# Kernel optimization log

Measured on AMD Instinct MI355X. Metric: run time of the kernel, lower is better.

## Reference

```python
import jax, jax.numpy as jnp
import numpy as np
from jax.scipy.special import logsumexp

N_ITERS = 20


def setup_inputs() -> dict:
    key = jax.random.key(0)
    k1, _ = jax.random.split(key)
    cost_matrix = jax.random.uniform(k1, (64, 1024, 1024), dtype=jnp.float32)
    epsilon = jnp.ones((1,), dtype=jnp.float32)
    return {"cost_matrix": cost_matrix, "epsilon": epsilon}


def reference(cost_matrix, epsilon):
    # log-space Sinkhorn: alternate row / column normalization in log domain
    log_alpha = -cost_matrix / epsilon  # (B, N, N)

    def step(la, _):
        la = la - logsumexp(la, axis=-1, keepdims=True)  # row normalize
        la = la - logsumexp(la, axis=-2, keepdims=True)  # col normalize
        return la, None

    log_alpha, _ = jax.lax.scan(step, log_alpha, None, length=N_ITERS)
    return jnp.exp(log_alpha)
```

## Files before the change

### kernel.cpp

```cpp
#include <hip/hip_runtime.h>
#include <hip/hip_fp16.h>


#define BATCH 64
#define N 1024
#define NITERS 20
#define ROWS_PER_BLOCK 64
#define BLOCKS_PER_BATCH (N / ROWS_PER_BLOCK)
#define THREADS 256
#define NU2 (N / 4)
#define NU4 (N / 8)
#define NU4F8 (N / 16)

typedef float f32x2 __attribute__((ext_vector_type(2)));

union H2U { __half2 h; unsigned u; };

__device__ __forceinline__ float4 h4_to_f4(uint2 r) {
    H2U a, b;
    a.u = r.x; b.u = r.y;
    float2 fa = __half22float2(a.h);
    float2 fb = __half22float2(b.h);
    return make_float4(fa.x, fa.y, fb.x, fb.y);
}

__device__ __forceinline__ void h8_unpack(uint4 r, float* f) {
    H2U a, b, c, d;
    a.u = r.x; b.u = r.y; c.u = r.z; d.u = r.w;
    float2 fa = __half22float2(a.h), fb = __half22float2(b.h);
    float2 fc = __half22float2(c.h), fd = __half22float2(d.h);
    f[0] = fa.x; f[1] = fa.y; f[2] = fb.x; f[3] = fb.y;
    f[4] = fc.x; f[5] = fc.y; f[6] = fd.x; f[7] = fd.y;
}

__device__ __forceinline__ uint4 h8_pack(const float* f) {
    H2U a, b, c, d;
    a.h = __float22half2_rn(make_float2(f[0], f[1]));
    b.h = __float22half2_rn(make_float2(f[2], f[3]));
    c.h = __float22half2_rn(make_float2(f[4], f[5]));
    d.h = __float22half2_rn(make_float2(f[6], f[7]));
    uint4 r; r.x = a.u; r.y = b.u; r.z = c.u; r.w = d.u;
    return r;
}

__device__ __forceinline__ uint4 pack_fp8_16(const float* k) {
    uint4 r;
    int a;
    a = __builtin_amdgcn_cvt_pk_fp8_f32(k[0],  k[1],  0, false);
    a = __builtin_amdgcn_cvt_pk_fp8_f32(k[2],  k[3],  a, true);
    r.x = (unsigned)a;
    a = __builtin_amdgcn_cvt_pk_fp8_f32(k[4],  k[5],  0, false);
    a = __builtin_amdgcn_cvt_pk_fp8_f32(k[6],  k[7],  a, true);
    r.y = (unsigned)a;
    a = __builtin_amdgcn_cvt_pk_fp8_f32(k[8],  k[9],  0, false);
    a = __builtin_amdgcn_cvt_pk_fp8_f32(k[10], k[11], a, true);
    r.z = (unsigned)a;
    a = __builtin_amdgcn_cvt_pk_fp8_f32(k[12], k[13], 0, false);
    a = __builtin_amdgcn_cvt_pk_fp8_f32(k[14], k[15], a, true);
    r.w = (unsigned)a;
    return r;
}

__device__ __forceinline__ void unpack_fp8_16(uint4 r, float* f) {
    f32x2 p;
    p = __builtin_amdgcn_cvt_pk_f32_fp8((int)r.x, false); f[0]  = p.x; f[1]  = p.y;
    p = __builtin_amdgcn_cvt_pk_f32_fp8((int)r.x, true);  f[2]  = p.x; f[3]  = p.y;
    p = __builtin_amdgcn_cvt_pk_f32_fp8((int)r.y, false); f[4]  = p.x; f[5]  = p.y;
    p = __builtin_amdgcn_cvt_pk_f32_fp8((int)r.y, true);  f[6]  = p.x; f[7]  = p.y;
    p = __builtin_amdgcn_cvt_pk_f32_fp8((int)r.z, false); f[8]  = p.x; f[9]  = p.y;
    p = __builtin_amdgcn_cvt_pk_f32_fp8((int)r.z, true);  f[10] = p.x; f[11] = p.y;
    p = __builtin_amdgcn_cvt_pk_f32_fp8((int)r.w, false); f[12] = p.x; f[13] = p.y;
    p = __builtin_amdgcn_cvt_pk_f32_fp8((int)r.w, true);  f[14] = p.x; f[15] = p.y;
}


__global__ __launch_bounds__(THREADS) void sk_zero(float* __restrict__ csum_all) {
    const int i = blockIdx.x * THREADS + threadIdx.x;
    csum_all[i] = 0.0f;
}

__global__ __launch_bounds__(THREADS) void sk_build(
        const float* __restrict__ C, const float* __restrict__ eps,
        uint4* __restrict__ K16, uint4* __restrict__ K8,
        float* __restrict__ u, float* __restrict__ csum_out) {
    __shared__ float4 smc[4][N / 4];
    const int t = threadIdx.x;
    const int lane = t & 63, w = t >> 6;
    const int b = blockIdx.y;
    const int row0 = blockIdx.x * ROWS_PER_BLOCK + w * 16;
    const float nie = -1.0f / eps[0];

    const float4* __restrict__ Cp =
        (const float4*)(C + ((size_t)b * N + row0) * N) + lane * 4;
    uint4* __restrict__ Kp16 = K16 + ((size_t)b * N + row0) * NU4 + lane * 2;
    uint4* __restrict__ Kp8  = K8  + ((size_t)b * N + row0) * NU4F8 + lane;

    float colacc[16];
    #pragma unroll
    for (int q = 0; q < 16; ++q) colacc[q] = 0.0f;

    float4 cur[4];
    #pragma unroll
    for (int q = 0; q < 4; ++q) cur[q] = Cp[q];

    for (int i = 0; i < 16; ++i) {
        float4 nxt[4];
        if (i < 15) {
            #pragma unroll
            for (int q = 0; q < 4; ++q) nxt[q] = Cp[(i + 1) * (N / 4) + q];
        }
        float k[16];
        const float* cf = (const float*)cur;
        #pragma unroll
        for (int q = 0; q < 16; ++q) k[q] = __expf(cf[q] * nie);

        Kp16[(size_t)i * NU4]     = h8_pack(k);
        Kp16[(size_t)i * NU4 + 1] = h8_pack(k + 8);
        Kp8[(size_t)i * NU4F8]    = pack_fp8_16(k);

        float s = (((k[0] + k[1]) + (k[2] + k[3])) + ((k[4] + k[5]) + (k[6] + k[7])))
                + (((k[8] + k[9]) + (k[10] + k[11])) + ((k[12] + k[13]) + (k[14] + k[15])));
        #pragma unroll
        for (int off = 32; off; off >>= 1) s += __shfl_xor(s, off, 64);
        const float ui = 1.0f / s;
        if (lane == 0) u[b * N + row0 + i] = ui;

        #pragma unroll
        for (int q = 0; q < 16; ++q) colacc[q] += k[q] * ui;

        if (i < 15) {
            #pragma unroll
            for (int q = 0; q < 4; ++q) cur[q] = nxt[q];
        }
    }

    #pragma unroll
    for (int q = 0; q < 4; ++q)
        smc[w][lane * 4 + q] = make_float4(colacc[4 * q], colacc[4 * q + 1],
                                           colacc[4 * q + 2], colacc[4 * q + 3]);
    __syncthreads();
    float4 s0 = smc[0][t], s1 = smc[1][t], s2 = smc[2][t], s3 = smc[3][t];
    float4 sum;
    sum.x = (s0.x + s1.x) + (s2.x + s3.x);
    sum.y = (s0.y + s1.y) + (s2.y + s3.y);
    sum.z = (s0.z + s1.z) + (s2.z + s3.z);
    sum.w = (s0.w + s1.w) + (s2.w + s3.w);
    float* cs = csum_out + b * N + 4 * t;
    atomicAdd(cs + 0, sum.x);
    atomicAdd(cs + 1, sum.y);
    atomicAdd(cs + 2, sum.z);
    atomicAdd(cs + 3, sum.w);
}

__global__ __launch_bounds__(THREADS) void sk_iter8(
        const uint4* __restrict__ K8, const float* __restrict__ csum_in,
        float* __restrict__ csum_out) {
    __shared__ float4 smc[4][N / 4];
    const int t = threadIdx.x;
    const int lane = t & 63, w = t >> 6;
    const int b = blockIdx.y;
    const int row0 = blockIdx.x * ROWS_PER_BLOCK + w * 16;

    const float4* __restrict__ cin = (const float4*)(csum_in + b * N) + lane * 4;
    float vv[16];
    #pragma unroll
    for (int q = 0; q < 4; ++q) {
        float4 c = cin[q];
        vv[4 * q + 0] = 1.0f / c.x;
        vv[4 * q + 1] = 1.0f / c.y;
        vv[4 * q + 2] = 1.0f / c.z;
        vv[4 * q + 3] = 1.0f / c.w;
    }

    const uint4* __restrict__ Kp = K8 + ((size_t)b * N + row0) * NU4F8 + lane;

    float colacc[16];
    #pragma unroll
    for (int q = 0; q < 16; ++q) colacc[q] = 0.0f;

    uint4 c0 = Kp[0];
    uint4 c1 = Kp[NU4F8];
    for (int i = 0; i < 16; ++i) {
        uint4 c2;
        if (i < 14) c2 = Kp[(size_t)(i + 2) * NU4F8];

        float k[16];
        unpack_fp8_16(c0, k);

        float pa = (k[0] * vv[0] + k[1] * vv[1]) + (k[2] * vv[2] + k[3] * vv[3]);
        float pb = (k[4] * vv[4] + k[5] * vv[5]) + (k[6] * vv[6] + k[7] * vv[7]);
        float pc = (k[8] * vv[8] + k[9] * vv[9]) + (k[10] * vv[10] + k[11] * vv[11]);
        float pd = (k[12] * vv[12] + k[13] * vv[13]) + (k[14] * vv[14] + k[15] * vv[15]);
        float s = (pa + pb) + (pc + pd);

        #pragma unroll
        for (int off = 32; off; off >>= 1) s += __shfl_xor(s, off, 64);
        const float ui = 1.0f / s;

        #pragma unroll
        for (int q = 0; q < 16; ++q) colacc[q] += k[q] * ui;

        c0 = c1;
        if (i < 14) c1 = c2;
    }

    #pragma unroll
    for (int q = 0; q < 4; ++q)
        smc[w][lane * 4 + q] = make_float4(colacc[4 * q], colacc[4 * q + 1],
                                           colacc[4 * q + 2], colacc[4 * q + 3]);
    __syncthreads();
    float4 s0 = smc[0][t], s1 = smc[1][t], s2 = smc[2][t], s3 = smc[3][t];
    float4 sum;
    sum.x = (s0.x + s1.x) + (s2.x + s3.x);
    sum.y = (s0.y + s1.y) + (s2.y + s3.y);
    sum.z = (s0.z + s1.z) + (s2.z + s3.z);
    sum.w = (s0.w + s1.w) + (s2.w + s3.w);
    float* cs = csum_out + b * N + 4 * t;
    atomicAdd(cs + 0, sum.x);
    atomicAdd(cs + 1, sum.y);
    atomicAdd(cs + 2, sum.z);
    atomicAdd(cs + 3, sum.w);
}

__global__ __launch_bounds__(THREADS) void sk_iter(
        const uint4* __restrict__ K, const float* __restrict__ csum_in,
        float* __restrict__ u, float* __restrict__ csum_out) {
    __shared__ float4 smc[4][N / 4];
    const int t = threadIdx.x;
    const int lane = t & 63, w = t >> 6;
    const int b = blockIdx.y;
    const int row0 = blockIdx.x * ROWS_PER_BLOCK + w * 16;

    const float4* __restrict__ cin = (const float4*)(csum_in + b * N) + lane * 4;
    float vv[16];
    #pragma unroll
    for (int q = 0; q < 4; ++q) {
        float4 c = cin[q];
        vv[4 * q + 0] = 1.0f / c.x;
        vv[4 * q + 1] = 1.0f / c.y;
        vv[4 * q + 2] = 1.0f / c.z;
        vv[4 * q + 3] = 1.0f / c.w;
    }

    const uint4* __restrict__ Kp = K + ((size_t)b * N + row0) * NU4 + lane * 2;

    float colacc[16];
    #pragma unroll
    for (int q = 0; q < 16; ++q) colacc[q] = 0.0f;

    uint4 c0 = Kp[0], c1 = Kp[1];
    for (int i = 0; i < 16; ++i) {
        uint4 n0, n1;
        if (i < 15) {
            n0 = Kp[(size_t)(i + 1) * NU4];
            n1 = Kp[(size_t)(i + 1) * NU4 + 1];
        }
        float k[16];
        h8_unpack(c0, k);
        h8_unpack(c1, k + 8);

        float pa = (k[0] * vv[0] + k[1] * vv[1]) + (k[2] * vv[2] + k[3] * vv[3]);
        float pb = (k[4] * vv[4] + k[5] * vv[5]) + (k[6] * vv[6] + k[7] * vv[7]);
        float pc = (k[8] * vv[8] + k[9] * vv[9]) + (k[10] * vv[10] + k[11] * vv[11]);
        float pd = (k[12] * vv[12] + k[13] * vv[13]) + (k[14] * vv[14] + k[15] * vv[15]);
        float s = (pa + pb) + (pc + pd);

        #pragma unroll
        for (int off = 32; off; off >>= 1) s += __shfl_xor(s, off, 64);
        const float ui = 1.0f / s;
        if (lane == 0) u[b * N + row0 + i] = ui;

        #pragma unroll
        for (int q = 0; q < 16; ++q) colacc[q] += k[q] * ui;

        if (i < 15) { c0 = n0; c1 = n1; }
    }

    #pragma unroll
    for (int q = 0; q < 4; ++q)
        smc[w][lane * 4 + q] = make_float4(colacc[4 * q], colacc[4 * q + 1],
                                           colacc[4 * q + 2], colacc[4 * q + 3]);
    __syncthreads();
    float4 s0 = smc[0][t], s1 = smc[1][t], s2 = smc[2][t], s3 = smc[3][t];
    float4 sum;
    sum.x = (s0.x + s1.x) + (s2.x + s3.x);
    sum.y = (s0.y + s1.y) + (s2.y + s3.y);
    sum.z = (s0.z + s1.z) + (s2.z + s3.z);
    sum.w = (s0.w + s1.w) + (s2.w + s3.w);
    float* cs = csum_out + b * N + 4 * t;
    atomicAdd(cs + 0, sum.x);
    atomicAdd(cs + 1, sum.y);
    atomicAdd(cs + 2, sum.z);
    atomicAdd(cs + 3, sum.w);
}

__global__ __launch_bounds__(THREADS) void sk_final(
        const uint2* __restrict__ K, const float* __restrict__ u,
        const float* __restrict__ csum_last, float* __restrict__ out) {
    const int t = threadIdx.x;
    const int row = blockIdx.x;
    const int b = blockIdx.y;
    const float ui = u[b * N + row];
    const float4 ci = ((const float4*)(csum_last + b * N))[t];
    const float4 vv = make_float4(1.0f / ci.x, 1.0f / ci.y, 1.0f / ci.z, 1.0f / ci.w);
    const size_t base = (size_t)b * N + row;
    float4 k = h4_to_f4((K + base * NU2)[t]);
    float4 o;
    o.x = k.x * ui * vv.x;
    o.y = k.y * ui * vv.y;
    o.z = k.z * ui * vv.z;
    o.w = k.w * ui * vv.w;
    ((float4*)(out + base * N))[t] = o;
}


__device__ __forceinline__ float block_reduce_broadcast(float val, float* lds) {
    #pragma unroll
    for (int off = 32; off > 0; off >>= 1)
        val += __shfl_xor(val, off, 64);
    const int lane = threadIdx.x & 63;
    const int wid  = threadIdx.x >> 6;
    if (lane == 0) lds[wid] = val;
    __syncthreads();
    float total = lds[0] + lds[1] + lds[2] + lds[3];
    __syncthreads();
    return total;
}

__global__ __launch_bounds__(THREADS) void sink_init(float* __restrict__ v,
                                                     float* __restrict__ colsum) {
    const int i = blockIdx.x * THREADS + threadIdx.x;
    v[i] = 1.0f;
    colsum[i] = 0.0f;
}

__global__ __launch_bounds__(THREADS) void sink_iter(
        const float* __restrict__ C, const float* __restrict__ eps,
        const float* __restrict__ v, float* __restrict__ u,
        float* __restrict__ colsum) {
    __shared__ float lds[4];
    const int t = threadIdx.x;
    const int b = blockIdx.y;
    const int row0 = blockIdx.x * ROWS_PER_BLOCK;
    const float neg_inv_eps = -1.0f / eps[0];

    const float4 vv = ((const float4*)(v + b * N))[t];
    const float4* __restrict__ Cp = (const float4*)(C + ((size_t)b * N + row0) * N);

    float4 colacc = make_float4(0.f, 0.f, 0.f, 0.f);
    float4 cur = Cp[t];
    for (int i = 0; i < ROWS_PER_BLOCK; ++i) {
        float4 nxt = cur;
        if (i + 1 < ROWS_PER_BLOCK)
            nxt = Cp[(size_t)(i + 1) * (N / 4) + t];

        float4 k;
        k.x = __expf(cur.x * neg_inv_eps);
        k.y = __expf(cur.y * neg_inv_eps);
        k.z = __expf(cur.z * neg_inv_eps);
        k.w = __expf(cur.w * neg_inv_eps);

        float s = k.x * vv.x + k.y * vv.y + k.z * vv.z + k.w * vv.w;
        float S = block_reduce_broadcast(s, lds);
        float ui = 1.0f / S;
        if (t == 0) u[b * N + row0 + i] = ui;

        colacc.x += k.x * ui;
        colacc.y += k.y * ui;
        colacc.z += k.z * ui;
        colacc.w += k.w * ui;
        cur = nxt;
    }

    float* cs = colsum + b * N + 4 * t;
    atomicAdd(cs + 0, colacc.x);
    atomicAdd(cs + 1, colacc.y);
    atomicAdd(cs + 2, colacc.z);
    atomicAdd(cs + 3, colacc.w);
}

__global__ __launch_bounds__(THREADS) void sink_fix(float* __restrict__ v,
                                                    float* __restrict__ colsum) {
    const int i = blockIdx.x * THREADS + threadIdx.x;
    v[i] = 1.0f / colsum[i];
    colsum[i] = 0.0f;
}

__global__ __launch_bounds__(THREADS) void sink_final(
        const float* __restrict__ C, const float* __restrict__ eps,
        const float* __restrict__ u, const float* __restrict__ v,
        float* __restrict__ out) {
    const int t = threadIdx.x;
    const int row = blockIdx.x;
    const int b = blockIdx.y;
    const float neg_inv_eps = -1.0f / eps[0];
    const float ui = u[b * N + row];
    const float4 vv = ((const float4*)(v + b * N))[t];
    const size_t base = ((size_t)b * N + row) * N;
    float4 c = ((const float4*)(C + base))[t];
    float4 o;
    o.x = __expf(c.x * neg_inv_eps) * ui * vv.x;
    o.y = __expf(c.y * neg_inv_eps) * ui * vv.y;
    o.z = __expf(c.z * neg_inv_eps) * ui * vv.z;
    o.w = __expf(c.w * neg_inv_eps) * ui * vv.w;
    ((float4*)(out + base))[t] = o;
}


extern "C" void kernel_launch(void* const* d_in, const int* in_sizes, int n_in,
                              void* d_out, int out_size, void* d_ws, size_t ws_size,
                              hipStream_t stream) {
    const float* C   = (const float*)d_in[0];
    const float* eps = (const float*)d_in[1];
    float* out = (float*)d_out;

    const size_t k16_bytes = (size_t)BATCH * N * N * 2;
    const size_t k8_bytes  = (size_t)BATCH * N * N;
    const size_t uv_elems  = (size_t)BATCH * N;
    const size_t needed    = k16_bytes + k8_bytes + uv_elems * 4 * (1 + NITERS);

    if (ws_size >= needed) {
        uint4* K16 = (uint4*)d_ws;
        uint4* K8  = (uint4*)((char*)d_ws + k16_bytes);
        float* u   = (float*)((char*)d_ws + k16_bytes + k8_bytes);
        float* csum = u + uv_elems;

        sk_zero<<<dim3(NITERS * uv_elems / THREADS), dim3(THREADS), 0, stream>>>(csum);
        sk_build<<<dim3(BLOCKS_PER_BATCH, BATCH), dim3(THREADS), 0, stream>>>(
            C, eps, K16, K8, u, csum);
        for (int it = 2; it <= NITERS - 1; ++it) {
            sk_iter8<<<dim3(BLOCKS_PER_BATCH, BATCH), dim3(THREADS), 0, stream>>>(
                K8, csum + (size_t)(it - 2) * uv_elems,
                csum + (size_t)(it - 1) * uv_elems);
        }
        sk_iter<<<dim3(BLOCKS_PER_BATCH, BATCH), dim3(THREADS), 0, stream>>>(
            K16, csum + (size_t)(NITERS - 2) * uv_elems, u,
            csum + (size_t)(NITERS - 1) * uv_elems);
        sk_final<<<dim3(N, BATCH), dim3(THREADS), 0, stream>>>(
            (const uint2*)K16, u, csum + (size_t)(NITERS - 1) * uv_elems, out);
    } else {
        float* u      = (float*)d_ws;
        float* v      = u + uv_elems;
        float* colsum = v + uv_elems;
        sink_init<<<dim3(BATCH * N / THREADS), dim3(THREADS), 0, stream>>>(v, colsum);
        for (int it = 0; it < NITERS; ++it) {
            sink_iter<<<dim3(BLOCKS_PER_BATCH, BATCH), dim3(THREADS), 0, stream>>>(
                C, eps, v, u, colsum);
            sink_fix<<<dim3(BATCH * N / THREADS), dim3(THREADS), 0, stream>>>(v, colsum);
        }
        sink_final<<<dim3(N, BATCH), dim3(THREADS), 0, stream>>>(C, eps, u, v, out);
    }
}
```

Baseline: 1.006 ms.

## Fuse all Sinkhorn stages into one persistent kernel with grid barriers

```diff
diff --git a/kernel.cpp b/kernel.cpp
--- a/kernel.cpp
+++ b/kernel.cpp
@@ -5,12 +5,16 @@
 #define BATCH 64
 #define N 1024
 #define NITERS 20
-#define ROWS_PER_BLOCK 64
-#define BLOCKS_PER_BATCH (N / ROWS_PER_BLOCK)
+#define RPB 64
+#define BPB 16
+#define NBLK (BATCH * BPB)
 #define THREADS 256
 #define NU2 (N / 4)
 #define NU4 (N / 8)
 #define NU4F8 (N / 16)
+#define NGRP 64
+#define CSUM_ELEMS ((size_t)NITERS * BATCH * N)
+#define BAR_WORDS 128
 
 typedef float f32x2 __attribute__((ext_vector_type(2)));
 
@@ -73,11 +77,262 @@
     p = __builtin_amdgcn_cvt_pk_f32_fp8((int)r.w, true);  f[14] = p.x; f[15] = p.y;
 }
 
-
-__global__ __launch_bounds__(THREADS) void sk_zero(float* __restrict__ csum_all) {
+__global__ __launch_bounds__(THREADS) void sk_zero(float* __restrict__ csum_all,
+                                                   int total) {
     const int i = blockIdx.x * THREADS + threadIdx.x;
-    csum_all[i] = 0.0f;
-}
+    if (i < total) csum_all[i] = 0.0f;
+}
+
+__device__ __forceinline__ void gbar(unsigned* __restrict__ bar,
+                                     unsigned& gencount) {
+    __syncthreads();
+    if (threadIdx.x == 0) {
+        __threadfence();
+        unsigned* grp    = bar;
+        unsigned* master = bar + NGRP;
+        unsigned* gen    = bar + NGRP + 1;
+        const unsigned gid = blockIdx.x & (NGRP - 1);
+        if (atomicAdd(&grp[gid], 1u) == (NBLK / NGRP) - 1u) {
+            if (atomicAdd(master, 1u) == NGRP - 1u) {
+                #pragma unroll
+                for (int i = 0; i < NGRP; ++i) atomicExch(&grp[i], 0u);
+                atomicExch(master, 0u);
+                __threadfence();
+                atomicAdd(gen, 1u);
+            }
+        }
+        while (__hip_atomic_load(gen, __ATOMIC_RELAXED,
+                                 __HIP_MEMORY_SCOPE_AGENT) == gencount)
+            __builtin_amdgcn_s_sleep(2);
+        __threadfence();
+    }
+    __syncthreads();
+    ++gencount;
+}
+
+__global__ __launch_bounds__(THREADS, 4) void sk_fused(
+        const float* __restrict__ C, const float* __restrict__ eps,
+        uint4* __restrict__ K16, uint4* __restrict__ K8,
+        float* __restrict__ csum, unsigned* __restrict__ bar,
+        float* __restrict__ out) {
+    __shared__ float4 smc[4][N / 4];
+    __shared__ float u_lds[RPB];
+    const int t = threadIdx.x;
+    const int lane = t & 63, w = t >> 6;
+    const int bid = blockIdx.x;
+    const int b = bid >> 4, bx = bid & 15;
+    const int row0 = bx * RPB + w * 16;
+    const int tt = (t + 16 * bx) & 255;
+    unsigned gencount = 0;
+
+    {
+        const float nie = -1.0f / eps[0];
+        const float4* __restrict__ Cp =
+            (const float4*)(C + ((size_t)b * N + row0) * N) + lane * 4;
+        uint4* __restrict__ Kp16 = K16 + ((size_t)b * N + row0) * NU4 + lane * 2;
+        uint4* __restrict__ Kp8  = K8  + ((size_t)b * N + row0) * NU4F8 + lane;
+
+        float colacc[16];
+        #pragma unroll
+        for (int q = 0; q < 16; ++q) colacc[q] = 0.0f;
+
+        float4 cur[4];
+        #pragma unroll
+        for (int q = 0; q < 4; ++q) cur[q] = Cp[q];
+
+        #pragma unroll
+        for (int i = 0; i < 16; ++i) {
+            float4 nxt[4];
+            if (i < 15) {
+                #pragma unroll
+                for (int q = 0; q < 4; ++q) nxt[q] = Cp[(i + 1) * (N / 4) + q];
+            }
+            float k[16];
+            const float* cf = (const float*)cur;
+            #pragma unroll
+            for (int q = 0; q < 16; ++q) k[q] = __expf(cf[q] * nie);
+
+            Kp16[(size_t)i * NU4]     = h8_pack(k);
+            Kp16[(size_t)i * NU4 + 1] = h8_pack(k + 8);
+            Kp8[(size_t)i * NU4F8]    = pack_fp8_16(k);
+
+            float s = (((k[0] + k[1]) + (k[2] + k[3])) + ((k[4] + k[5]) + (k[6] + k[7])))
+                    + (((k[8] + k[9]) + (k[10] + k[11])) + ((k[12] + k[13]) + (k[14] + k[15])));
+            #pragma unroll
+            for (int off = 32; off; off >>= 1) s += __shfl_xor(s, off, 64);
+            const float ui = 1.0f / s;
+
+            #pragma unroll
+            for (int q = 0; q < 16; ++q) colacc[q] += k[q] * ui;
+
+            if (i < 15) {
+                #pragma unroll
+                for (int q = 0; q < 4; ++q) cur[q] = nxt[q];
+            }
+        }
+
+        #pragma unroll
+        for (int q = 0; q < 4; ++q)
+            smc[w][lane * 4 + q] = make_float4(colacc[4 * q], colacc[4 * q + 1],
+                                               colacc[4 * q + 2], colacc[4 * q + 3]);
+        __syncthreads();
+        float4 s0 = smc[0][tt], s1 = smc[1][tt], s2 = smc[2][tt], s3 = smc[3][tt];
+        float* cs = csum + b * N + 4 * tt;
+        atomicAdd(cs + 0, (s0.x + s1.x) + (s2.x + s3.x));
+        atomicAdd(cs + 1, (s0.y + s1.y) + (s2.y + s3.y));
+        atomicAdd(cs + 2, (s0.z + s1.z) + (s2.z + s3.z));
+        atomicAdd(cs + 3, (s0.w + s1.w) + (s2.w + s3.w));
+    }
+    gbar(bar, gencount);
+
+    const uint4* __restrict__ Kp8r = K8 + ((size_t)b * N + row0) * NU4F8 + lane;
+    #pragma unroll 1
+    for (int p = 1; p <= 18; ++p) {
+        const float4* __restrict__ cin =
+            (const float4*)(csum + (size_t)(p - 1) * BATCH * N + b * N) + lane * 4;
+        float vv[16];
+        #pragma unroll
+        for (int q = 0; q < 4; ++q) {
+            float4 c = cin[q];
+            vv[4 * q + 0] = 1.0f / c.x;
+            vv[4 * q + 1] = 1.0f / c.y;
+            vv[4 * q + 2] = 1.0f / c.z;
+            vv[4 * q + 3] = 1.0f / c.w;
+        }
+
+        float colacc[16];
+        #pragma unroll
+        for (int q = 0; q < 16; ++q) colacc[q] = 0.0f;
+
+        uint4 buf[4];
+        #pragma unroll
+        for (int q = 0; q < 4; ++q) buf[q] = Kp8r[(size_t)q * NU4F8];
+
+        __syncthreads();
+        #pragma unroll
+        for (int i = 0; i < 16; ++i) {
+            uint4 nx;
+            if (i < 12) nx = Kp8r[(size_t)(i + 4) * NU4F8];
+
+            float k[16];
+            unpack_fp8_16(buf[i & 3], k);
+
+            float pa = (k[0] * vv[0] + k[1] * vv[1]) + (k[2] * vv[2] + k[3] * vv[3]);
+            float pb = (k[4] * vv[4] + k[5] * vv[5]) + (k[6] * vv[6] + k[7] * vv[7]);
+            float pc = (k[8] * vv[8] + k[9] * vv[9]) + (k[10] * vv[10] + k[11] * vv[11]);
+            float pd = (k[12] * vv[12] + k[13] * vv[13]) + (k[14] * vv[14] + k[15] * vv[15]);
+            float s = (pa + pb) + (pc + pd);
+
+            #pragma unroll
+            for (int off = 32; off; off >>= 1) s += __shfl_xor(s, off, 64);
+            const float ui = 1.0f / s;
+
+            #pragma unroll
+            for (int q = 0; q < 16; ++q) colacc[q] += k[q] * ui;
+
+            if (i < 12) buf[i & 3] = nx;
+        }
+
+        #pragma unroll
+        for (int q = 0; q < 4; ++q)
+            smc[w][lane * 4 + q] = make_float4(colacc[4 * q], colacc[4 * q + 1],
+                                               colacc[4 * q + 2], colacc[4 * q + 3]);
+        __syncthreads();
+        float4 s0 = smc[0][tt], s1 = smc[1][tt], s2 = smc[2][tt], s3 = smc[3][tt];
+        float* cs = csum + (size_t)p * BATCH * N + b * N + 4 * tt;
+        atomicAdd(cs + 0, (s0.x + s1.x) + (s2.x + s3.x));
+        atomicAdd(cs + 1, (s0.y + s1.y) + (s2.y + s3.y));
+        atomicAdd(cs + 2, (s0.z + s1.z) + (s2.z + s3.z));
+        atomicAdd(cs + 3, (s0.w + s1.w) + (s2.w + s3.w));
+        gbar(bar, gencount);
+    }
+
+    {
+        const float4* __restrict__ cin =
+            (const float4*)(csum + (size_t)18 * BATCH * N + b * N) + lane * 4;
+        float vv[16];
+        #pragma unroll
+        for (int q = 0; q < 4; ++q) {
+            float4 c = cin[q];
+            vv[4 * q + 0] = 1.0f / c.x;
+            vv[4 * q + 1] = 1.0f / c.y;
+            vv[4 * q + 2] = 1.0f / c.z;
+            vv[4 * q + 3] = 1.0f / c.w;
+        }
+
+        const uint4* __restrict__ Kp = K16 + ((size_t)b * N + row0) * NU4 + lane * 2;
+
+        float colacc[16];
+        #pragma unroll
+        for (int q = 0; q < 16; ++q) colacc[q] = 0.0f;
+
+        uint4 c0 = Kp[0], c1 = Kp[1];
+        #pragma unroll
+        for (int i = 0; i < 16; ++i) {
+            uint4 n0, n1;
+            if (i < 15) {
+                n0 = Kp[(size_t)(i + 1) * NU4];
+                n1 = Kp[(size_t)(i + 1) * NU4 + 1];
+            }
+            float k[16];
+            h8_unpack(c0, k);
+            h8_unpack(c1, k + 8);
+
+            float pa = (k[0] * vv[0] + k[1] * vv[1]) + (k[2] * vv[2] + k[3] * vv[3]);
+            float pb = (k[4] * vv[4] + k[5] * vv[5]) + (k[6] * vv[6] + k[7] * vv[7]);
+            float pc = (k[8] * vv[8] + k[9] * vv[9]) + (k[10] * vv[10] + k[11] * vv[11]);
+            float pd = (k[12] * vv[12] + k[13] * vv[13]) + (k[14] * vv[14] + k[15] * vv[15]);
+            float s = (pa + pb) + (pc + pd);
+
+            #pragma unroll
+            for (int off = 32; off; off >>= 1) s += __shfl_xor(s, off, 64);
+            const float ui = 1.0f / s;
+            if (lane == 0) u_lds[w * 16 + i] = ui;
+
+            #pragma unroll
+            for (int q = 0; q < 16; ++q) colacc[q] += k[q] * ui;
+
+            if (i < 15) { c0 = n0; c1 = n1; }
+        }
+
+        #pragma unroll
+        for (int q = 0; q < 4; ++q)
+            smc[w][lane * 4 + q] = make_float4(colacc[4 * q], colacc[4 * q + 1],
+                                               colacc[4 * q + 2], colacc[4 * q + 3]);
+        __syncthreads();
+        float4 s0 = smc[0][tt], s1 = smc[1][tt], s2 = smc[2][tt], s3 = smc[3][tt];
+        float* cs = csum + (size_t)19 * BATCH * N + b * N + 4 * tt;
+        atomicAdd(cs + 0, (s0.x + s1.x) + (s2.x + s3.x));
+        atomicAdd(cs + 1, (s0.y + s1.y) + (s2.y + s3.y));
+        atomicAdd(cs + 2, (s0.z + s1.z) + (s2.z + s3.z));
+        atomicAdd(cs + 3, (s0.w + s1.w) + (s2.w + s3.w));
+    }
+    gbar(bar, gencount);
+
+    {
+        const float4 ci = ((const float4*)(csum + (size_t)19 * BATCH * N + b * N))[t];
+        const float4 vv = make_float4(1.0f / ci.x, 1.0f / ci.y,
+                                      1.0f / ci.z, 1.0f / ci.w);
+        const size_t rowbase = (size_t)b * N + (size_t)bx * RPB;
+        const uint2* __restrict__ K2 = (const uint2*)K16;
+
+        uint2 kc = K2[rowbase * NU2 + t];
+        for (int r = 0; r < RPB; ++r) {
+            uint2 kn;
+            if (r < RPB - 1) kn = K2[(rowbase + r + 1) * NU2 + t];
+            const float ur = u_lds[r];
+            float4 k = h4_to_f4(kc);
+            float4 o;
+            o.x = k.x * ur * vv.x;
+            o.y = k.y * ur * vv.y;
+            o.z = k.z * ur * vv.z;
+            o.w = k.w * ur * vv.w;
+            ((float4*)(out + (rowbase + r) * N))[t] = o;
+            kc = kn;
+        }
+    }
+}
+
 
 __global__ __launch_bounds__(THREADS) void sk_build(
         const float* __restrict__ C, const float* __restrict__ eps,
@@ -87,7 +342,7 @@
     const int t = threadIdx.x;
     const int lane = t & 63, w = t >> 6;
     const int b = blockIdx.y;
-    const int row0 = blockIdx.x * ROWS_PER_BLOCK + w * 16;
+    const int row0 = blockIdx.x * RPB + w * 16;
     const float nie = -1.0f / eps[0];
 
     const float4* __restrict__ Cp =
@@ -140,16 +395,11 @@
                                            colacc[4 * q + 2], colacc[4 * q + 3]);
     __syncthreads();
     float4 s0 = smc[0][t], s1 = smc[1][t], s2 = smc[2][t], s3 = smc[3][t];
-    float4 sum;
-    sum.x = (s0.x + s1.x) + (s2.x + s3.x);
-    sum.y = (s0.y + s1.y) + (s2.y + s3.y);
-    sum.z = (s0.z + s1.z) + (s2.z + s3.z);
-    sum.w = (s0.w + s1.w) + (s2.w + s3.w);
     float* cs = csum_out + b * N + 4 * t;
-    atomicAdd(cs + 0, sum.x);
-    atomicAdd(cs + 1, sum.y);
-    atomicAdd(cs + 2, sum.z);
-    atomicAdd(cs + 3, sum.w);
+    atomicAdd(cs + 0, (s0.x + s1.x) + (s2.x + s3.x));
+    atomicAdd(cs + 1, (s0.y + s1.y) + (s2.y + s3.y));
+    atomicAdd(cs + 2, (s0.z + s1.z) + (s2.z + s3.z));
+    atomicAdd(cs + 3, (s0.w + s1.w) + (s2.w + s3.w));
 }
 
 __global__ __launch_bounds__(THREADS) void sk_iter8(
@@ -159,7 +409,7 @@
     const int t = threadIdx.x;
     const int lane = t & 63, w = t >> 6;
     const int b = blockIdx.y;
-    const int row0 = blockIdx.x * ROWS_PER_BLOCK + w * 16;
+    const int row0 = blockIdx.x * RPB + w * 16;
 
     const float4* __restrict__ cin = (const float4*)(csum_in + b * N) + lane * 4;
     float vv[16];
@@ -210,16 +460,11 @@
                                            colacc[4 * q + 2], colacc[4 * q + 3]);
     __syncthreads();
     float4 s0 = smc[0][t], s1 = smc[1][t], s2 = smc[2][t], s3 = smc[3][t];
-    float4 sum;
-    sum.x = (s0.x + s1.x) + (s2.x + s3.x);
-    sum.y = (s0.y + s1.y) + (s2.y + s3.y);
-    sum.z = (s0.z + s1.z) + (s2.z + s3.z);
-    sum.w = (s0.w + s1.w) + (s2.w + s3.w);
     float* cs = csum_out + b * N + 4 * t;
-    atomicAdd(cs + 0, sum.x);
-    atomicAdd(cs + 1, sum.y);
-    atomicAdd(cs + 2, sum.z);
-    atomicAdd(cs + 3, sum.w);
+    atomicAdd(cs + 0, (s0.x + s1.x) + (s2.x + s3.x));
+    atomicAdd(cs + 1, (s0.y + s1.y) + (s2.y + s3.y));
+    atomicAdd(cs + 2, (s0.z + s1.z) + (s2.z + s3.z));
+    atomicAdd(cs + 3, (s0.w + s1.w) + (s2.w + s3.w));
 }
 
 __global__ __launch_bounds__(THREADS) void sk_iter(
@@ -229,7 +474,7 @@
     const int t = threadIdx.x;
     const int lane = t & 63, w = t >> 6;
     const int b = blockIdx.y;
-    const int row0 = blockIdx.x * ROWS_PER_BLOCK + w * 16;
+    const int row0 = blockIdx.x * RPB + w * 16;
 
     const float4* __restrict__ cin = (const float4*)(csum_in + b * N) + lane * 4;
     float vv[16];
@@ -282,16 +527,11 @@
                                            colacc[4 * q + 2], colacc[4 * q + 3]);
     __syncthreads();
     float4 s0 = smc[0][t], s1 = smc[1][t], s2 = smc[2][t], s3 = smc[3][t];
-    float4 sum;
-    sum.x = (s0.x + s1.x) + (s2.x + s3.x);
-    sum.y = (s0.y + s1.y) + (s2.y + s3.y);
-    sum.z = (s0.z + s1.z) + (s2.z + s3.z);
-    sum.w = (s0.w + s1.w) + (s2.w + s3.w);
     float* cs = csum_out + b * N + 4 * t;
-    atomicAdd(cs + 0, sum.x);
-    atomicAdd(cs + 1, sum.y);
-    atomicAdd(cs + 2, sum.z);
-    atomicAdd(cs + 3, sum.w);
+    atomicAdd(cs + 0, (s0.x + s1.x) + (s2.x + s3.x));
+    atomicAdd(cs + 1, (s0.y + s1.y) + (s2.y + s3.y));
+    atomicAdd(cs + 2, (s0.z + s1.z) + (s2.z + s3.z));
+    atomicAdd(cs + 3, (s0.w + s1.w) + (s2.w + s3.w));
 }
 
 __global__ __launch_bounds__(THREADS) void sk_final(
@@ -341,7 +581,7 @@
     __shared__ float lds[4];
     const int t = threadIdx.x;
     const int b = blockIdx.y;
-    const int row0 = blockIdx.x * ROWS_PER_BLOCK;
+    const int row0 = blockIdx.x * RPB;
     const float neg_inv_eps = -1.0f / eps[0];
 
     const float4 vv = ((const float4*)(v + b * N))[t];
@@ -349,9 +589,9 @@
 
     float4 colacc = make_float4(0.f, 0.f, 0.f, 0.f);
     float4 cur = Cp[t];
-    for (int i = 0; i < ROWS_PER_BLOCK; ++i) {
+    for (int i = 0; i < RPB; ++i) {
         float4 nxt = cur;
-        if (i + 1 < ROWS_PER_BLOCK)
+        if (i + 1 < RPB)
             nxt = Cp[(size_t)(i + 1) * (N / 4) + t];
 
         float4 k;
@@ -417,34 +657,52 @@
     const size_t k16_bytes = (size_t)BATCH * N * N * 2;
     const size_t k8_bytes  = (size_t)BATCH * N * N;
     const size_t uv_elems  = (size_t)BATCH * N;
-    const size_t needed    = k16_bytes + k8_bytes + uv_elems * 4 * (1 + NITERS);
+    const size_t needed    = k16_bytes + k8_bytes +
+                             (CSUM_ELEMS + BAR_WORDS + uv_elems) * 4;
 
     if (ws_size >= needed) {
         uint4* K16 = (uint4*)d_ws;
         uint4* K8  = (uint4*)((char*)d_ws + k16_bytes);
-        float* u   = (float*)((char*)d_ws + k16_bytes + k8_bytes);
-        float* csum = u + uv_elems;
-
-        sk_zero<<<dim3(NITERS * uv_elems / THREADS), dim3(THREADS), 0, stream>>>(csum);
-        sk_build<<<dim3(BLOCKS_PER_BATCH, BATCH), dim3(THREADS), 0, stream>>>(
-            C, eps, K16, K8, u, csum);
-        for (int it = 2; it <= NITERS - 1; ++it) {
-            sk_iter8<<<dim3(BLOCKS_PER_BATCH, BATCH), dim3(THREADS), 0, stream>>>(
-                K8, csum + (size_t)(it - 2) * uv_elems,
-                csum + (size_t)(it - 1) * uv_elems);
-        }
-        sk_iter<<<dim3(BLOCKS_PER_BATCH, BATCH), dim3(THREADS), 0, stream>>>(
-            K16, csum + (size_t)(NITERS - 2) * uv_elems, u,
-            csum + (size_t)(NITERS - 1) * uv_elems);
-        sk_final<<<dim3(N, BATCH), dim3(THREADS), 0, stream>>>(
-            (const uint2*)K16, u, csum + (size_t)(NITERS - 1) * uv_elems, out);
+        float* csum = (float*)((char*)d_ws + k16_bytes + k8_bytes);
+        unsigned* bar = (unsigned*)(csum + CSUM_ELEMS);
+        float* u = (float*)(bar + BAR_WORDS);
+
+        static int coop_ok = -1;
+        if (coop_ok < 0) {
+            int nb = 0;
+            hipError_t e = hipOccupancyMaxActiveBlocksPerMultiprocessor(
+                &nb, sk_fused, THREADS, 0);
+            coop_ok = (e == hipSuccess && nb >= 4) ? 1 : 0;
+        }
+
+        const int zero_total = (int)(CSUM_ELEMS + BAR_WORDS);
+        sk_zero<<<dim3((zero_total + THREADS - 1) / THREADS), dim3(THREADS),
+                  0, stream>>>(csum, zero_total);
+
+        if (coop_ok) {
+            sk_fused<<<dim3(NBLK), dim3(THREADS), 0, stream>>>(
+                C, eps, K16, K8, csum, bar, out);
+        } else {
+            sk_build<<<dim3(BPB, BATCH), dim3(THREADS), 0, stream>>>(
+                C, eps, K16, K8, u, csum);
+            for (int it = 2; it <= NITERS - 1; ++it) {
+                sk_iter8<<<dim3(BPB, BATCH), dim3(THREADS), 0, stream>>>(
+                    K8, csum + (size_t)(it - 2) * uv_elems,
+                    csum + (size_t)(it - 1) * uv_elems);
+            }
+            sk_iter<<<dim3(BPB, BATCH), dim3(THREADS), 0, stream>>>(
+                K16, csum + (size_t)(NITERS - 2) * uv_elems, u,
+                csum + (size_t)(NITERS - 1) * uv_elems);
+            sk_final<<<dim3(N, BATCH), dim3(THREADS), 0, stream>>>(
+                (const uint2*)K16, u, csum + (size_t)(NITERS - 1) * uv_elems, out);
+        }
     } else {
         float* u      = (float*)d_ws;
         float* v      = u + uv_elems;
         float* colsum = v + uv_elems;
         sink_init<<<dim3(BATCH * N / THREADS), dim3(THREADS), 0, stream>>>(v, colsum);
         for (int it = 0; it < NITERS; ++it) {
-            sink_iter<<<dim3(BLOCKS_PER_BATCH, BATCH), dim3(THREADS), 0, stream>>>(
+            sink_iter<<<dim3(BPB, BATCH), dim3(THREADS), 0, stream>>>(
                 C, eps, v, u, colsum);
             sink_fix<<<dim3(BATCH * N / THREADS), dim3(THREADS), 0, stream>>>(v, colsum);
         }
```

Result: no change. 1.002 ms (-0.4%).
